# Performance work log

Measured on AMD Instinct MI355X. Metric: run time of the kernel, lower is better.

The kernel has to match this reference:

```python
import jax, jax.numpy as jnp
import numpy as np

B, S, C, H = 2, 2048, 1024, 16
D = C // H  # head_size = 64


def setup_inputs() -> dict:
    key = jax.random.key(0)
    ks = jax.random.split(key, 8)
    scale = 1.0 / np.sqrt(C)
    return {
        "src": jax.random.normal(ks[0], (B, S, C), dtype=jnp.float32),
        "Wq": jax.random.normal(ks[1], (C, C), dtype=jnp.float32) * scale,
        "bq": jnp.zeros((C,), dtype=jnp.float32),
        "Wk": jax.random.normal(ks[2], (C, C), dtype=jnp.float32) * scale,
        "bk": jnp.zeros((C,), dtype=jnp.float32),
        "Wv": jax.random.normal(ks[3], (C, C), dtype=jnp.float32) * scale,
        "bv": jnp.zeros((C,), dtype=jnp.float32),
        "rel_k_table": jax.random.normal(ks[4], (2 * S - 1, D), dtype=jnp.float32),
    }


def reference(src, Wq, bq, Wk, bk, Wv, bv, rel_k_table):
    # Linear projections (torch Linear: x @ W.T + b)
    q = src @ Wq.T + bq  # (B,S,C)
    k = src @ Wk.T + bk
    v = src @ Wv.T + bv
    # Faithful to torch .view: raw reshape (B,S,C) -> (B,H,S,D), NOT a transpose split
    q = q.reshape(B, H, S, D)
    k = k.reshape(B, H, S, D)
    v = v.reshape(B, H, S, D)
    # content score: q @ k^T
    content = jnp.einsum("bhsd,bhtd->bhst", q, k)  # (B,H,S,S)
    # relative-position embeddings: (S,S,D)
    pos = jnp.arange(S)
    shifted = pos[None, :] - pos[:, None] + (S - 1)  # (S,S) in [0, 2S-2]
    rel_k = rel_k_table[shifted]  # (S,S,D)
    # q.view(S, B*H, D) @ rel_k.permute(0,2,1): batched over first (query-pos) axis
    q_r = q.reshape(S, B * H, D)
    pos_score = jnp.einsum("sbd,std->sbt", q_r, rel_k)  # (S,BH,S)
    pos_score = jnp.transpose(pos_score, (1, 0, 2)).reshape(B, H, S, S)
    scores = (content + pos_score) / jnp.sqrt(jnp.float32(D))
    attn = jax.nn.softmax(scores, axis=-1)
    out = jnp.einsum("bhst,bhtd->bhsd", attn, v)  # (B,H,S,D)
    out = jnp.transpose(out, (0, 2, 1, 3)).reshape(B, S, C)
    return out
```

## Files before the change

### kernel.cpp

```cpp
#include <hip/hip_runtime.h>
#include <hip/hip_bf16.h>

#define BATCH 2
#define SEQ   2048
#define CH    1024
#define NH    16
#define HD    64
#define BHN   (BATCH*NH)
#define SD    (SEQ*HD)

typedef short v8s __attribute__((ext_vector_type(8)));
typedef short v4s __attribute__((ext_vector_type(4)));
typedef float v4f __attribute__((ext_vector_type(4)));

#define VMCNT2() asm volatile("s_waitcnt vmcnt(2)" ::: "memory")
#define VMCNT0() asm volatile("s_waitcnt vmcnt(0)" ::: "memory")
#define SBAR()  do { __builtin_amdgcn_sched_barrier(0); \
                     __builtin_amdgcn_s_barrier();      \
                     __builtin_amdgcn_sched_barrier(0); } while (0)

__device__ __forceinline__ short f2bf(float f) {
    unsigned u = __float_as_uint(f);
    u += 0x7fff + ((u >> 16) & 1);
    return (short)(u >> 16);
}

__device__ __forceinline__ unsigned pk2bf(float a, float b) {
    __hip_bfloat162 h = __float22bfloat162_rn(make_float2(a, b));
    unsigned u;
    __builtin_memcpy(&u, &h, 4);
    return u;
}

__device__ __forceinline__ float ex2(float x) {
    float r; asm("v_exp_f32 %0, %1" : "=v"(r) : "v"(x)); return r;
}

#if __has_builtin(__builtin_amdgcn_perm)
#define PERMB(a, b, s) __builtin_amdgcn_perm((a), (b), (s))
#else
__device__ __forceinline__ unsigned PERMB(unsigned a, unsigned b, unsigned s) {
    unsigned r = 0;
#pragma unroll
    for (int i = 0; i < 4; i++) {
        unsigned sb = (s >> (8 * i)) & 0xff, byte;
        if (sb >= 12) byte = (sb == 12) ? 0u : 0xffu;
        else if (sb < 4) byte = (b >> (8 * sb)) & 0xff;
        else byte = (a >> (8 * (sb - 4))) & 0xff;
        r |= byte << (8 * i);
    }
    return r;
}
#endif

__device__ __forceinline__ void gl_lds16(const short* g, short* l) {
    __builtin_amdgcn_global_load_lds(
        (const __attribute__((address_space(1))) void*)g,
        (__attribute__((address_space(3))) void*)l, 16, 0, 0);
}

__global__ __launch_bounds__(256) void cast_all_kernel(
    const float* __restrict__ src, const float* __restrict__ wq,
    const float* __restrict__ wk, const float* __restrict__ wv,
    const float* __restrict__ rel,
    short* __restrict__ xb, short* __restrict__ wqb,
    short* __restrict__ wkb, short* __restrict__ wvb,
    short* __restrict__ relb)
{
    const int z = blockIdx.z;
    const float* s; short* d; int n4;
    switch (z) {
        case 0: s = src; d = xb;   n4 = 1048576; break;
        case 1: s = wq;  d = wqb;  n4 = 262144;  break;
        case 2: s = wk;  d = wkb;  n4 = 262144;  break;
        case 3: s = wv;  d = wvb;  n4 = 262144;  break;
        default: s = rel; d = relb; n4 = 65520;  break;
    }
    for (int i = blockIdx.x * 256 + threadIdx.x; i < n4; i += gridDim.x * 256) {
        float4 v = ((const float4*)s)[i];
        v4s o; o.x = f2bf(v.x); o.y = f2bf(v.y); o.z = f2bf(v.z); o.w = f2bf(v.w);
        ((v4s*)d)[i] = o;
    }
}

__global__ __launch_bounds__(256, 3) void proj_mfma_kernel(
    const short* __restrict__ Xb,
    const short* __restrict__ Wqb, const short* __restrict__ Wkb,
    const short* __restrict__ Wvb,
    const float* __restrict__ bq, const float* __restrict__ bk,
    const float* __restrict__ bv,
    short* __restrict__ qo, short* __restrict__ ko, short* __restrict__ vo)
{
    const int z = blockIdx.z;
    const short* W    = (z == 0) ? Wqb : (z == 1) ? Wkb : Wvb;
    const float* bias = (z == 0) ? bq  : (z == 1) ? bk  : bv;
    short*       out  = (z == 0) ? qo  : (z == 1) ? ko  : vo;
    const float  osc  = (z == 0) ? 0.125f * 1.44269504088896f : 1.0f;

    const int m0 = blockIdx.x * 128;
    const int n0 = blockIdx.y * 128;
    const int tid  = threadIdx.x;
    const int w    = tid >> 6;
    const int lane = tid & 63;
    const int l15  = lane & 15;
    const int quad = lane >> 4;
    const int wm = w & 1, wn = w >> 1;

    __shared__ short Al[128 * 32];
    __shared__ short Bl[128 * 32];

    v4f acc[4][4];
#pragma unroll
    for (int i = 0; i < 4; i++)
#pragma unroll
        for (int j = 0; j < 4; j++) acc[i][j] = (v4f)(0.f);

    const int lr = lane >> 2;
    const int lc = (lane & 3) * 8;

    for (int k0 = 0; k0 < 1024; k0 += 32) {
        __syncthreads();
#pragma unroll
        for (int l = 0; l < 2; l++) {
            const int slab = w * 32 + l * 16;
            gl_lds16(Xb + (size_t)(m0 + slab + lr) * 1024 + k0 + lc,
                     &Al[slab * 32]);
            gl_lds16(W + (size_t)(n0 + slab + lr) * 1024 + k0 + lc,
                     &Bl[slab * 32]);
        }
        __syncthreads();
        v8s af[4], bf[4];
#pragma unroll
        for (int mt = 0; mt < 4; mt++)
            af[mt] = *(const v8s*)&Al[(wm * 64 + mt * 16 + l15) * 32 + quad * 8];
#pragma unroll
        for (int nt = 0; nt < 4; nt++)
            bf[nt] = *(const v8s*)&Bl[(wn * 64 + nt * 16 + l15) * 32 + quad * 8];
#pragma unroll
        for (int mt = 0; mt < 4; mt++)
#pragma unroll
            for (int nt = 0; nt < 4; nt++)
                acc[mt][nt] = __builtin_amdgcn_mfma_f32_16x16x32_bf16(
                    af[mt], bf[nt], acc[mt][nt], 0, 0, 0);
    }

    float bv4[4];
#pragma unroll
    for (int nt = 0; nt < 4; nt++)
        bv4[nt] = bias[n0 + wn * 64 + nt * 16 + l15];
#pragma unroll
    for (int mt = 0; mt < 4; mt++)
#pragma unroll
        for (int rg = 0; rg < 4; rg++) {
            const int row = m0 + wm * 64 + mt * 16 + quad * 4 + rg;
#pragma unroll
            for (int nt = 0; nt < 4; nt++)
                out[(size_t)row * 1024 + n0 + wn * 64 + nt * 16 + l15] =
                    f2bf((acc[mt][nt][rg] + bv4[nt]) * osc);
        }
}

__global__ __launch_bounds__(256) void vtrans_kernel(
    const short* __restrict__ v, short* __restrict__ vt)
{
    const int bh = blockIdx.y;
    const int t0 = blockIdx.x * 64;
    const int r = threadIdx.x >> 3;
    const int c = (threadIdx.x & 7) * 8;

    __shared__ short T[64][72];
    *(v8s*)&T[r][c] =
        *(const v8s*)(v + (size_t)bh * SD + (size_t)(t0 + r) * HD + c);
    *(v8s*)&T[r + 32][c] =
        *(const v8s*)(v + (size_t)bh * SD + (size_t)(t0 + r + 32) * HD + c);
    __syncthreads();
    v8s o0, o1;
#pragma unroll
    for (int e = 0; e < 8; e++) {
        const int t = 2 * (threadIdx.x & 7) + (e >> 2) + 16 * (e & 3);
        o0[e] = T[t][r];
        o1[e] = T[t][r + 32];
    }
    *(v8s*)(vt + (size_t)bh * SD + (size_t)r * SEQ + t0 + c) = o0;
    *(v8s*)(vt + (size_t)bh * SD + (size_t)(r + 32) * SEQ + t0 + c) = o1;
}

__global__ __launch_bounds__(256, 2) void attn_mfma_kernel(
    const short* __restrict__ qb, const short* __restrict__ kb,
    const short* __restrict__ vtb, const short* __restrict__ relb,
    float* __restrict__ out)
{
    const int tid  = threadIdx.x;
    const int w    = tid >> 6;
    const int lane = tid & 63;
    const int l15  = lane & 15;
    const int quad = lane >> 4;
    const int bh = blockIdx.x, b = bh >> 4, h = bh & 15;
    const int s0 = blockIdx.y * 128;
    const int i0 = w * 32;

    __shared__ short Kl[2][64][64];
    __shared__ short Vl[2][64][64];
    __shared__ short Rl[256][64];
    __shared__ short Pb[4][2][16][64];

    v8s qc_f[2][2], qr_f[2][2];
#pragma unroll
    for (int mt = 0; mt < 2; mt++)
#pragma unroll
    for (int kh = 0; kh < 2; kh++) {
        const int row = s0 + i0 + mt * 16 + l15;
        qc_f[mt][kh] = *(const v8s*)(qb + (size_t)bh * SD +
                                     (size_t)row * HD + kh * 32 + quad * 8);
        qr_f[mt][kh] = *(const v8s*)(qb + (size_t)row * (BHN * HD) +
                                     bh * HD + kh * 32 + quad * 8);
    }

    int      slv4[4];
    unsigned selA[4], selB[4], pwoff[4];
#pragma unroll
    for (int rg = 0; rg < 4; rg++) {
        const int ii = quad * 4 + rg;
        const int e  = l15 + 15 - ii;
        const bool lo = (e < 16);
        slv4[rg] = (quad * 16 + (e & 15)) << 2;
        selA[rg] = lo ? 0x05040c0cu : 0x07060c0cu;
        selB[rg] = lo ? 0x07060c0cu : 0x01000c0cu;
        pwoff[rg] = (unsigned)(w * 4096 + ii * 128 +
                    ((((l15 >> 1) ^ (ii & 7)) << 4) + ((l15 & 1) << 3)));
    }

    const int swz = (quad ^ (l15 & 7)) << 4;
    int kaddr[2][4];
#pragma unroll
    for (int kh = 0; kh < 2; kh++) {
        const int x = kh << 6;
#pragma unroll
        for (int nt = 0; nt < 4; nt++)
            kaddr[kh][nt] = (((nt * 16 + l15) << 7) + swz) ^ x;
    }
    const int paddr0 = (l15 << 7) + swz;

    const int Bq = 1920 - s0;
    int raddr[6];
#pragma unroll
    for (int st = 0; st < 6; st++) {
        const int lg = 2032 - s0 - i0 - 16 + st * 16 + l15;
        raddr[st] = ((lg & 255) << 7) + ((quad ^ (lg & 7)) << 4);
    }

    const int strow = tid >> 3;
    const int stc   = ((tid & 7) ^ (strow & 7)) * 8;
    const short* ksrc = kb  + (size_t)bh * SD + (size_t)strow * HD  + stc;
    const short* vsrc = vtb + (size_t)bh * SD + (size_t)strow * SEQ + stc;

#pragma unroll
    for (int g = 0; g < 3; g++) {
        const int r0 = Bq + g * 64 + strow;
        const int ra = r0 < 4094 ? r0 : 4094;
        const int rb2 = (r0 + 32) < 4094 ? (r0 + 32) : 4094;
        const unsigned sl = (unsigned)((Bq + g * 64 + w * 8) & 255) << 7;
        gl_lds16(relb + (size_t)ra * HD + stc, (short*)((char*)Rl + sl));
        gl_lds16(relb + (size_t)rb2 * HD + stc, (short*)((char*)Rl + sl + 4096));
    }
    gl_lds16(ksrc,              &Kl[0][w * 8][0]);
    gl_lds16(ksrc + 32 * HD,    &Kl[0][32 + w * 8][0]);
    gl_lds16(vsrc,              &Vl[0][w * 8][0]);
    gl_lds16(vsrc + 32 * SEQ,   &Vl[0][32 + w * 8][0]);

    const short* kp = ksrc + 4096;
    const short* vp = vsrc + 64;
    const char*  relbp = (const char*)relb + stc * 2;
    unsigned roff = (unsigned)(Bq + 192 + strow) * 128;
    const unsigned ROMAX = 4094u * 128;
    unsigned rlds = (unsigned)((Bq + 192 + w * 8) & 255) << 7;

    v4f o_acc[2][4];
#pragma unroll
    for (int mt = 0; mt < 2; mt++)
#pragma unroll
        for (int nt = 0; nt < 4; nt++) o_acc[mt][nt] = (v4f)(0.f);
    float lpart[2][4] = {{0.f,0.f,0.f,0.f},{0.f,0.f,0.f,0.f}};

    const v4f vz = (v4f)(0.f);

    v4f cacc[2][4], racc[2][5];
    unsigned g01[2][4], g23[2][4], g4v[2][4];

    auto STAGE_K = [&](int dst) {
        short* kd = &Kl[0][w * 8][0] + (dst << 12);
        gl_lds16(kp,            kd);
        gl_lds16(kp + 32 * HD,  kd + 32 * 64);
        unsigned rc0 = roff < ROMAX ? roff : ROMAX;
        unsigned rc1 = (roff + 4096) < ROMAX ? (roff + 4096) : ROMAX;
        gl_lds16((const short*)(relbp + rc0), (short*)((char*)Rl + rlds));
        gl_lds16((const short*)(relbp + rc1), (short*)((char*)Rl + rlds + 4096));
        kp += 4096; roff += 8192; rlds = (rlds + 8192) & 32767;
    };

    auto STAGE_V = [&](int dst) {
        short* vd = &Vl[0][w * 8][0] + (dst << 12);
        gl_lds16(vp,            vd);
        gl_lds16(vp + 32 * SEQ, vd + 32 * 64);
        vp += 64;
    };

    auto QK = [&](int cur) {
        const char* kbase = (const char*)Kl + cur * 8192;
        const char* rbase = (const char*)Rl;
        {
            v8s kf[4], rfj[6];
#pragma unroll
            for (int nt = 0; nt < 4; nt++)
                kf[nt] = *(const v8s*)(kbase + kaddr[0][nt]);
#pragma unroll
            for (int st = 0; st < 6; st++)
                rfj[st] = *(const v8s*)(rbase + raddr[st]);
            __builtin_amdgcn_s_setprio(1);
#pragma unroll
            for (int mt = 0; mt < 2; mt++)
#pragma unroll
                for (int nt = 0; nt < 4; nt++)
                    cacc[mt][nt] = __builtin_amdgcn_mfma_f32_16x16x32_bf16(
                        qc_f[mt][0], kf[nt], vz, 0, 0, 0);
#pragma unroll
            for (int jt = 0; jt < 5; jt++)
                racc[0][jt] = __builtin_amdgcn_mfma_f32_16x16x32_bf16(
                    qr_f[0][0], rfj[jt + 1], vz, 0, 0, 0);
#pragma unroll
            for (int jt = 0; jt < 5; jt++)
                racc[1][jt] = __builtin_amdgcn_mfma_f32_16x16x32_bf16(
                    qr_f[1][0], rfj[jt], vz, 0, 0, 0);
            __builtin_amdgcn_s_setprio(0);
        }
        {
            v8s kf[4], rfj[6];
#pragma unroll
            for (int nt = 0; nt < 4; nt++)
                kf[nt] = *(const v8s*)(kbase + kaddr[1][nt]);
#pragma unroll
            for (int st = 0; st < 6; st++)
                rfj[st] = *(const v8s*)(rbase + (raddr[st] ^ 64));
            __builtin_amdgcn_s_setprio(1);
#pragma unroll
            for (int mt = 0; mt < 2; mt++)
#pragma unroll
                for (int nt = 0; nt < 4; nt++)
                    cacc[mt][nt] = __builtin_amdgcn_mfma_f32_16x16x32_bf16(
                        qc_f[mt][1], kf[nt], cacc[mt][nt], 0, 0, 0);
#pragma unroll
            for (int jt = 0; jt < 5; jt++)
                racc[0][jt] = __builtin_amdgcn_mfma_f32_16x16x32_bf16(
                    qr_f[0][1], rfj[jt + 1], racc[0][jt], 0, 0, 0);
#pragma unroll
            for (int jt = 0; jt < 5; jt++)
                racc[1][jt] = __builtin_amdgcn_mfma_f32_16x16x32_bf16(
                    qr_f[1][1], rfj[jt], racc[1][jt], 0, 0, 0);
            __builtin_amdgcn_s_setprio(0);
        }
#pragma unroll
        for (int st = 0; st < 6; st++) raddr[st] = (raddr[st] + 8192) & 32767;
    };

    auto PHASE1 = [&]() {
#pragma unroll
        for (int mt = 0; mt < 2; mt++)
#pragma unroll
        for (int rg = 0; rg < 4; rg++) {
            unsigned p01 = pk2bf(racc[mt][0][rg], racc[mt][1][rg]);
            unsigned p23 = pk2bf(racc[mt][2][rg], racc[mt][3][rg]);
            unsigned p4  = pk2bf(racc[mt][4][rg], racc[mt][4][rg]);
            g01[mt][rg] = (unsigned)__builtin_amdgcn_ds_bpermute(slv4[rg], (int)p01);
            g23[mt][rg] = (unsigned)__builtin_amdgcn_ds_bpermute(slv4[rg], (int)p23);
            g4v[mt][rg] = (unsigned)__builtin_amdgcn_ds_bpermute(slv4[rg], (int)p4);
        }
    };

    auto PHASE2 = [&]() {
#pragma unroll
        for (int mt = 0; mt < 2; mt++)
#pragma unroll
        for (int rg = 0; rg < 4; rg++) {
            const unsigned a01 = g01[mt][rg], a23 = g23[mt][rg], a4 = g4v[mt][rg];
            unsigned pb0 = PERMB(a01, a01, selA[rg]);
            unsigned pb1 = PERMB(a01, a23, selB[rg]);
            unsigned pb2 = PERMB(a23, a23, selA[rg]);
            unsigned pb3 = PERMB(a23, a4,  selB[rg]);
            float p0 = ex2(cacc[mt][0][rg] + __uint_as_float(pb0));
            float p1 = ex2(cacc[mt][1][rg] + __uint_as_float(pb1));
            float p2 = ex2(cacc[mt][2][rg] + __uint_as_float(pb2));
            float p3 = ex2(cacc[mt][3][rg] + __uint_as_float(pb3));
            lpart[mt][rg] += (p0 + p1) + (p2 + p3);
            *(uint2*)((char*)Pb + pwoff[rg] + mt * 2048) =
                make_uint2(pk2bf(p0, p1), pk2bf(p2, p3));
        }
    };

    auto PV = [&](int vbuf) {
        const char* vbase = (const char*)Vl + vbuf * 8192;
        const char* pbW = (const char*)Pb + w * 4096;
#pragma unroll
        for (int kh = 0; kh < 2; kh++) {
            v8s vf[4];
#pragma unroll
            for (int nt = 0; nt < 4; nt++)
                vf[nt] = *(const v8s*)(vbase + kaddr[kh][nt]);
            v8s pa0 = *(const v8s*)(pbW + (paddr0 ^ (kh << 6)));
            v8s pa1 = *(const v8s*)(pbW + 2048 + (paddr0 ^ (kh << 6)));
            __builtin_amdgcn_s_setprio(1);
#pragma unroll
            for (int nt = 0; nt < 4; nt++)
                o_acc[0][nt] = __builtin_amdgcn_mfma_f32_16x16x32_bf16(
                    pa0, vf[nt], o_acc[0][nt], 0, 0, 0);
#pragma unroll
            for (int nt = 0; nt < 4; nt++)
                o_acc[1][nt] = __builtin_amdgcn_mfma_f32_16x16x32_bf16(
                    pa1, vf[nt], o_acc[1][nt], 0, 0, 0);
            __builtin_amdgcn_s_setprio(0);
        }
    };

    VMCNT0();
    SBAR();
    STAGE_K(1);
    QK(0); PHASE1();
    SBAR();
    STAGE_V(1);
    PHASE2();

    int cur = 0;
    for (int t0 = 64; t0 < SEQ; t0 += 64) {
        cur ^= 1;
        VMCNT2();
        SBAR();
        STAGE_K(cur ^ 1);
        QK(cur);
        PHASE1();
        PV(cur ^ 1);
        SBAR();
        STAGE_V(cur ^ 1);
        PHASE2();
    }
    VMCNT0();
    SBAR();
    PV(cur);

#pragma unroll
    for (int mt = 0; mt < 2; mt++)
#pragma unroll
    for (int rg = 0; rg < 4; rg++) {
        float rs = lpart[mt][rg];
#pragma unroll
        for (int off = 1; off < 16; off <<= 1)
            rs += __shfl_xor(rs, off);
        const float inv = 1.f / rs;
        const int row = s0 + i0 + mt * 16 + quad * 4 + rg;
        const size_t base = ((size_t)b * SEQ + row) * CH + h * HD;
#pragma unroll
        for (int nt = 0; nt < 4; nt++)
            out[base + nt * 16 + l15] = o_acc[mt][nt][rg] * inv;
    }
}

extern "C" void kernel_launch(void* const* d_in, const int* in_sizes, int n_in,
                              void* d_out, int out_size, void* d_ws, size_t ws_size,
                              hipStream_t stream)
{
    const float* src  = (const float*)d_in[0];
    const float* Wq   = (const float*)d_in[1];
    const float* bq   = (const float*)d_in[2];
    const float* Wk   = (const float*)d_in[3];
    const float* bk   = (const float*)d_in[4];
    const float* Wv   = (const float*)d_in[5];
    const float* bv   = (const float*)d_in[6];
    const float* relk = (const float*)d_in[7];
    float* out = (float*)d_out;

    const size_t nQKV = (size_t)BATCH * SEQ * CH;
    const size_t nW   = (size_t)CH * CH;
    short* qb   = (short*)d_ws;
    short* kb   = qb + nQKV;
    short* vb   = kb + nQKV;
    short* vtb  = vb + nQKV;
    short* xb   = vtb + nQKV;
    short* wqb  = xb + nQKV;
    short* wkb  = wqb + nW;
    short* wvb  = wkb + nW;
    short* relb = wvb + nW;

    cast_all_kernel<<<dim3(512, 1, 5), 256, 0, stream>>>(
        src, Wq, Wk, Wv, relk, xb, wqb, wkb, wvb, relb);

    dim3 gProj(4096 / 128, 1024 / 128, 3);
    proj_mfma_kernel<<<gProj, 256, 0, stream>>>(
        xb, wqb, wkb, wvb, bq, bk, bv, qb, kb, vb);

    dim3 gVt(SEQ / 64, BHN);
    vtrans_kernel<<<gVt, 256, 0, stream>>>(vb, vtb);

    dim3 gAttn(BHN, SEQ / 128);
    attn_mfma_kernel<<<gAttn, 256, 0, stream>>>(qb, kb, vtb, relb, out);
}
```

Baseline: 208.8 us.

## Widen projection GEMM K-tile with swizzled LDS and trim rel-pos bpermutes

The QKV projection GEMM now stages 64-wide K slices per iteration into an XOR-swizzled LDS layout. This halves the number of barrier pairs and is meant to avoid LDS bank conflicts on fragment reads. In the attention kernel, the relative-position shift selects the correct packed bf16 pair before the cross-lane bpermute instead of after it. That cuts three bpermutes per row group to two and replaces the byte-permute ops with shifts and masks. The cost is more LDS per GEMM block and a few extra pack/select instructions per row group.

```diff
diff --git a/kernel.cpp b/kernel.cpp
--- a/kernel.cpp
+++ b/kernel.cpp
@@ -35,23 +35,6 @@
 __device__ __forceinline__ float ex2(float x) {
     float r; asm("v_exp_f32 %0, %1" : "=v"(r) : "v"(x)); return r;
 }
-
-#if __has_builtin(__builtin_amdgcn_perm)
-#define PERMB(a, b, s) __builtin_amdgcn_perm((a), (b), (s))
-#else
-__device__ __forceinline__ unsigned PERMB(unsigned a, unsigned b, unsigned s) {
-    unsigned r = 0;
-#pragma unroll
-    for (int i = 0; i < 4; i++) {
-        unsigned sb = (s >> (8 * i)) & 0xff, byte;
-        if (sb >= 12) byte = (sb == 12) ? 0u : 0xffu;
-        else if (sb < 4) byte = (b >> (8 * sb)) & 0xff;
-        else byte = (a >> (8 * (sb - 4))) & 0xff;
-        r |= byte << (8 * i);
-    }
-    return r;
-}
-#endif
 
 __device__ __forceinline__ void gl_lds16(const short* g, short* l) {
     __builtin_amdgcn_global_load_lds(
@@ -106,8 +89,8 @@
     const int quad = lane >> 4;
     const int wm = w & 1, wn = w >> 1;
 
-    __shared__ short Al[128 * 32];
-    __shared__ short Bl[128 * 32];
+    __shared__ short Al[128 * 64];
+    __shared__ short Bl[128 * 64];
 
     v4f acc[4][4];
 #pragma unroll
@@ -115,33 +98,50 @@
 #pragma unroll
         for (int j = 0; j < 4; j++) acc[i][j] = (v4f)(0.f);
 
-    const int lr = lane >> 2;
-    const int lc = (lane & 3) * 8;
-
-    for (int k0 = 0; k0 < 1024; k0 += 32) {
+    const int srow = tid >> 3;
+    const int scol = ((tid & 7) ^ (srow & 7)) * 8;
+
+    int aoff[2][4], boff[2][4];
+#pragma unroll
+    for (int kk = 0; kk < 2; kk++) {
+#pragma unroll
+        for (int mt = 0; mt < 4; mt++) {
+            const int ra = wm * 64 + mt * 16 + l15;
+            aoff[kk][mt] = ra * 64 + ((((kk << 2) | quad) ^ (ra & 7)) << 3);
+        }
+#pragma unroll
+        for (int nt = 0; nt < 4; nt++) {
+            const int rb = wn * 64 + nt * 16 + l15;
+            boff[kk][nt] = rb * 64 + ((((kk << 2) | quad) ^ (rb & 7)) << 3);
+        }
+    }
+
+    for (int k0 = 0; k0 < 1024; k0 += 64) {
         __syncthreads();
 #pragma unroll
-        for (int l = 0; l < 2; l++) {
-            const int slab = w * 32 + l * 16;
-            gl_lds16(Xb + (size_t)(m0 + slab + lr) * 1024 + k0 + lc,
-                     &Al[slab * 32]);
-            gl_lds16(W + (size_t)(n0 + slab + lr) * 1024 + k0 + lc,
-                     &Bl[slab * 32]);
+        for (int j = 0; j < 4; j++) {
+            gl_lds16(Xb + (size_t)(m0 + j * 32 + srow) * 1024 + k0 + scol,
+                     &Al[(j * 32 + w * 8) * 64]);
+            gl_lds16(W + (size_t)(n0 + j * 32 + srow) * 1024 + k0 + scol,
+                     &Bl[(j * 32 + w * 8) * 64]);
         }
         __syncthreads();
-        v8s af[4], bf[4];
-#pragma unroll
-        for (int mt = 0; mt < 4; mt++)
-            af[mt] = *(const v8s*)&Al[(wm * 64 + mt * 16 + l15) * 32 + quad * 8];
-#pragma unroll
-        for (int nt = 0; nt < 4; nt++)
-            bf[nt] = *(const v8s*)&Bl[(wn * 64 + nt * 16 + l15) * 32 + quad * 8];
-#pragma unroll
-        for (int mt = 0; mt < 4; mt++)
-#pragma unroll
-            for (int nt = 0; nt < 4; nt++)
-                acc[mt][nt] = __builtin_amdgcn_mfma_f32_16x16x32_bf16(
-                    af[mt], bf[nt], acc[mt][nt], 0, 0, 0);
+#pragma unroll
+        for (int kk = 0; kk < 2; kk++) {
+            v8s af[4], bf4[4];
+#pragma unroll
+            for (int mt = 0; mt < 4; mt++)
+                af[mt] = *(const v8s*)&Al[aoff[kk][mt]];
+#pragma unroll
+            for (int nt = 0; nt < 4; nt++)
+                bf4[nt] = *(const v8s*)&Bl[boff[kk][nt]];
+#pragma unroll
+            for (int mt = 0; mt < 4; mt++)
+#pragma unroll
+                for (int nt = 0; nt < 4; nt++)
+                    acc[mt][nt] = __builtin_amdgcn_mfma_f32_16x16x32_bf16(
+                        af[mt], bf4[nt], acc[mt][nt], 0, 0, 0);
+        }
     }
 
     float bv4[4];
@@ -216,16 +216,15 @@
                                      bh * HD + kh * 32 + quad * 8);
     }
 
-    int      slv4[4];
-    unsigned selA[4], selB[4], pwoff[4];
+    int  slv4[4];
+    bool slo[4];
+    unsigned pwoff[4];
 #pragma unroll
     for (int rg = 0; rg < 4; rg++) {
         const int ii = quad * 4 + rg;
         const int e  = l15 + 15 - ii;
-        const bool lo = (e < 16);
         slv4[rg] = (quad * 16 + (e & 15)) << 2;
-        selA[rg] = lo ? 0x05040c0cu : 0x07060c0cu;
-        selB[rg] = lo ? 0x07060c0cu : 0x01000c0cu;
+        slo[rg]  = (l15 >= 15 - ii);
         pwoff[rg] = (unsigned)(w * 4096 + ii * 128 +
                     ((((l15 >> 1) ^ (ii & 7)) << 4) + ((l15 & 1) << 3)));
     }
@@ -285,7 +284,7 @@
     const v4f vz = (v4f)(0.f);
 
     v4f cacc[2][4], racc[2][5];
-    unsigned g01[2][4], g23[2][4], g4v[2][4];
+    unsigned g1v[2][4], g2v[2][4];
 
     auto STAGE_K = [&](int dst) {
         short* kd = &Kl[0][w * 8][0] + (dst << 12);
@@ -368,11 +367,13 @@
 #pragma unroll
         for (int rg = 0; rg < 4; rg++) {
             unsigned p01 = pk2bf(racc[mt][0][rg], racc[mt][1][rg]);
+            unsigned p12 = pk2bf(racc[mt][1][rg], racc[mt][2][rg]);
             unsigned p23 = pk2bf(racc[mt][2][rg], racc[mt][3][rg]);
-            unsigned p4  = pk2bf(racc[mt][4][rg], racc[mt][4][rg]);
-            g01[mt][rg] = (unsigned)__builtin_amdgcn_ds_bpermute(slv4[rg], (int)p01);
-            g23[mt][rg] = (unsigned)__builtin_amdgcn_ds_bpermute(slv4[rg], (int)p23);
-            g4v[mt][rg] = (unsigned)__builtin_amdgcn_ds_bpermute(slv4[rg], (int)p4);
+            unsigned p34 = pk2bf(racc[mt][3][rg], racc[mt][4][rg]);
+            unsigned q1 = slo[rg] ? p01 : p12;
+            unsigned q2 = slo[rg] ? p23 : p34;
+            g1v[mt][rg] = (unsigned)__builtin_amdgcn_ds_bpermute(slv4[rg], (int)q1);
+            g2v[mt][rg] = (unsigned)__builtin_amdgcn_ds_bpermute(slv4[rg], (int)q2);
         }
     };
 
@@ -381,11 +382,11 @@
         for (int mt = 0; mt < 2; mt++)
 #pragma unroll
         for (int rg = 0; rg < 4; rg++) {
-            const unsigned a01 = g01[mt][rg], a23 = g23[mt][rg], a4 = g4v[mt][rg];
-            unsigned pb0 = PERMB(a01, a01, selA[rg]);
-            unsigned pb1 = PERMB(a01, a23, selB[rg]);
-            unsigned pb2 = PERMB(a23, a23, selA[rg]);
-            unsigned pb3 = PERMB(a23, a4,  selB[rg]);
+            const unsigned a1 = g1v[mt][rg], a2 = g2v[mt][rg];
+            const unsigned pb0 = a1 << 16;
+            const unsigned pb1 = a1 & 0xffff0000u;
+            const unsigned pb2 = a2 << 16;
+            const unsigned pb3 = a2 & 0xffff0000u;
             float p0 = ex2(cacc[mt][0][rg] + __uint_as_float(pb0));
             float p1 = ex2(cacc[mt][1][rg] + __uint_as_float(pb1));
             float p2 = ex2(cacc[mt][2][rg] + __uint_as_float(pb2));
```

New measurement: 203.4 us. 1.03x faster.

## Double K-tile depth in QKV projection GEMM and XOR-swizzle LDS layout

Applied to the files above, without the earlier changes.

The QKV projection GEMM now stages 64-wide K slices per iteration instead of 32, which halves the number of barrier pairs per tile. It also applies an XOR swizzle to the LDS layout to avoid bank conflicts when fragments are read. Fragment offsets are precomputed outside the loop. The cost is double the LDS footprint per block, which may reduce occupancy, and this affects only the projection stage, not the attention kernel.

```diff
diff --git a/kernel.cpp b/kernel.cpp
--- a/kernel.cpp
+++ b/kernel.cpp
@@ -106,8 +106,8 @@
     const int quad = lane >> 4;
     const int wm = w & 1, wn = w >> 1;
 
-    __shared__ short Al[128 * 32];
-    __shared__ short Bl[128 * 32];
+    __shared__ short Al[128 * 64];
+    __shared__ short Bl[128 * 64];
 
     v4f acc[4][4];
 #pragma unroll
@@ -115,33 +115,50 @@
 #pragma unroll
         for (int j = 0; j < 4; j++) acc[i][j] = (v4f)(0.f);
 
-    const int lr = lane >> 2;
-    const int lc = (lane & 3) * 8;
-
-    for (int k0 = 0; k0 < 1024; k0 += 32) {
+    const int srow = tid >> 3;
+    const int scol = ((tid & 7) ^ (srow & 7)) * 8;
+
+    int aoff[2][4], boff[2][4];
+#pragma unroll
+    for (int kk = 0; kk < 2; kk++) {
+#pragma unroll
+        for (int mt = 0; mt < 4; mt++) {
+            const int ra = wm * 64 + mt * 16 + l15;
+            aoff[kk][mt] = ra * 64 + ((((kk << 2) | quad) ^ (ra & 7)) << 3);
+        }
+#pragma unroll
+        for (int nt = 0; nt < 4; nt++) {
+            const int rb = wn * 64 + nt * 16 + l15;
+            boff[kk][nt] = rb * 64 + ((((kk << 2) | quad) ^ (rb & 7)) << 3);
+        }
+    }
+
+    for (int k0 = 0; k0 < 1024; k0 += 64) {
         __syncthreads();
 #pragma unroll
-        for (int l = 0; l < 2; l++) {
-            const int slab = w * 32 + l * 16;
-            gl_lds16(Xb + (size_t)(m0 + slab + lr) * 1024 + k0 + lc,
-                     &Al[slab * 32]);
-            gl_lds16(W + (size_t)(n0 + slab + lr) * 1024 + k0 + lc,
-                     &Bl[slab * 32]);
+        for (int j = 0; j < 4; j++) {
+            gl_lds16(Xb + (size_t)(m0 + j * 32 + srow) * 1024 + k0 + scol,
+                     &Al[(j * 32 + w * 8) * 64]);
+            gl_lds16(W + (size_t)(n0 + j * 32 + srow) * 1024 + k0 + scol,
+                     &Bl[(j * 32 + w * 8) * 64]);
         }
         __syncthreads();
-        v8s af[4], bf[4];
-#pragma unroll
-        for (int mt = 0; mt < 4; mt++)
-            af[mt] = *(const v8s*)&Al[(wm * 64 + mt * 16 + l15) * 32 + quad * 8];
-#pragma unroll
-        for (int nt = 0; nt < 4; nt++)
-            bf[nt] = *(const v8s*)&Bl[(wn * 64 + nt * 16 + l15) * 32 + quad * 8];
-#pragma unroll
-        for (int mt = 0; mt < 4; mt++)
-#pragma unroll
-            for (int nt = 0; nt < 4; nt++)
-                acc[mt][nt] = __builtin_amdgcn_mfma_f32_16x16x32_bf16(
-                    af[mt], bf[nt], acc[mt][nt], 0, 0, 0);
+#pragma unroll
+        for (int kk = 0; kk < 2; kk++) {
+            v8s af[4], bf4[4];
+#pragma unroll
+            for (int mt = 0; mt < 4; mt++)
+                af[mt] = *(const v8s*)&Al[aoff[kk][mt]];
+#pragma unroll
+            for (int nt = 0; nt < 4; nt++)
+                bf4[nt] = *(const v8s*)&Bl[boff[kk][nt]];
+#pragma unroll
+            for (int mt = 0; mt < 4; mt++)
+#pragma unroll
+                for (int nt = 0; nt < 4; nt++)
+                    acc[mt][nt] = __builtin_amdgcn_mfma_f32_16x16x32_bf16(
+                        af[mt], bf4[nt], acc[mt][nt], 0, 0, 0);
+        }
     }
 
     float bv4[4];
```

Measured after the change: 215.4 us. 3.1% more time.
